# Kernel optimization log

Hardware: AMD Instinct MI355X
Metric: run time of the kernel (lower is better)

Reference implementation:

```python
import jax, jax.numpy as jnp
import numpy as np

EPS = 1e-6
B, H, S, D = 8, 16, 4096, 64


def setup_inputs() -> dict:
    key = jax.random.key(0)
    k1, k2, k3 = jax.random.split(key, 3)
    return {
        "keys": jax.random.normal(k1, (B, H, S, D), dtype=jnp.float32),
        "values": jax.random.normal(k2, (B, H, S, D), dtype=jnp.float32),
        "queries": jax.random.normal(k3, (B, H, S, D), dtype=jnp.float32),
    }


def reference(keys, values, queries):
    # update: accumulate outer-product associative memory per (batch, head)
    # M[b,h] = sum_s k_s outer v_s  -> [B, H, D, D]
    M = jnp.einsum("bhsd,bhse->bhde", keys, values)
    # normalizer z[b,h] = sum_s k_s -> [B, H, D]
    z = jnp.sum(keys, axis=2)
    # retrieve: out = (q @ M) / (q . z + eps)
    num = jnp.einsum("bhqd,bhde->bhqe", queries, M)        # [B, H, S, D]
    den = jnp.einsum("bhqd,bhd->bhq", queries, z) + EPS     # [B, H, S]
    return num / den[..., None]
```

## Files before the change

kernel.cpp:

```cpp
#include <hip/hip_runtime.h>

constexpr int Sc = 4096, Dc = 64;
constexpr int BH = 128;
constexpr int SS = 8;
constexpr int CHUNK = Sc / SS;
constexpr int SROWS = 32;
constexpr int NST = CHUNK / SROWS;
constexpr int MM = Dc * Dc;
constexpr int NZP = SS * 4;
constexpr int QT = 128;

using sh8 = __attribute__((ext_vector_type(8))) short;
using f32x4 = __attribute__((ext_vector_type(4))) float;
typedef __attribute__((address_space(1))) const unsigned int as1_u32;
typedef __attribute__((address_space(3))) unsigned int as3_u32;

__device__ __forceinline__ unsigned int packbf2(float lo, float hi) {
  unsigned int a = __builtin_bit_cast(unsigned int, lo);
  unsigned int b = __builtin_bit_cast(unsigned int, hi);
  a = (a + 0x7fffu + ((a >> 16) & 1u)) >> 16;
  b = (b + 0x7fffu + ((b >> 16) & 1u)) & 0xffff0000u;
  return a | b;
}

__global__ __launch_bounds__(256) void k1_accum(const float* __restrict__ K,
                                                const float* __restrict__ V,
                                                float* __restrict__ Pm,
                                                double* __restrict__ Pz) {
  const int blk = blockIdx.x, bh = blk >> 3, ck = blk & 7;
  const int tid = threadIdx.x, w = tid >> 6, l = tid & 63;
  const int g = l >> 4, c = l & 15;

  const size_t base = ((size_t)bh * Sc + (size_t)ck * CHUNK) * Dc;
  const float* Kg = K + base;
  const float* Vg = V + base;

  __shared__ __align__(16) float smem[2 * 4096];

  const int lofs = w * 512 + l * 4;

  f32x4 acc[4];
  #pragma unroll
  for (int i = 0; i < 4; ++i) acc[i] = (f32x4){0.f, 0.f, 0.f, 0.f};
  double zacc = 0.0;

#define K1_ISSUE(T, BUF)                                                         \
  {                                                                              \
    const float* gk_ = Kg + (size_t)(T) * 2048 + lofs;                           \
    const float* gv_ = Vg + (size_t)(T) * 2048 + lofs;                           \
    float* lk_ = &smem[(BUF) * 4096 + w * 512];           \
    float* lv_ = &smem[(BUF) * 4096 + 2048 + w * 512];                           \
    __builtin_amdgcn_global_load_lds((as1_u32*)gk_,         (as3_u32*)lk_,         16, 0, 0); \
    __builtin_amdgcn_global_load_lds((as1_u32*)(gk_ + 256), (as3_u32*)(lk_ + 256), 16, 0, 0); \
    __builtin_amdgcn_global_load_lds((as1_u32*)gv_,         (as3_u32*)lv_,         16, 0, 0); \
    __builtin_amdgcn_global_load_lds((as1_u32*)(gv_ + 256), (as3_u32*)(lv_ + 256), 16, 0, 0); \
  }

  K1_ISSUE(0, 0)

  for (int t = 0; t < NST; ++t) {
    const int buf = t & 1;
    asm volatile("s_waitcnt vmcnt(0)" ::: "memory");
    asm volatile("s_waitcnt lgkmcnt(0)" ::: "memory");
    __builtin_amdgcn_s_barrier();
    if (t + 1 < NST) K1_ISSUE(t + 1, buf ^ 1)

    const float* bK = &smem[buf * 4096];
    const float* bV = &smem[buf * 4096 + 2048];

    #pragma unroll
    for (int r = 0; r < 8; ++r) zacc += (double)bK[(8 * w + r) * 64 + l];

    float ak[8];
    #pragma unroll
    for (int j = 0; j < 8; ++j) ak[j] = bK[(8 * g + j) * 64 + 16 * w + c];
    unsigned int au[4];
    #pragma unroll
    for (int j = 0; j < 4; ++j) au[j] = packbf2(ak[2 * j], ak[2 * j + 1]);
    const sh8 afr = __builtin_bit_cast(sh8, *(const uint4*)au);

    #pragma unroll
    for (int et = 0; et < 4; ++et) {
      float bv[8];
      #pragma unroll
      for (int j = 0; j < 8; ++j) bv[j] = bV[(8 * g + j) * 64 + 16 * et + c];
      unsigned int bu[4];
      #pragma unroll
      for (int j = 0; j < 4; ++j) bu[j] = packbf2(bv[2 * j], bv[2 * j + 1]);
      const sh8 bfr = __builtin_bit_cast(sh8, *(const uint4*)bu);
      acc[et] = __builtin_amdgcn_mfma_f32_16x16x32_bf16(afr, bfr, acc[et], 0, 0, 0);
    }
  }
#undef K1_ISSUE

  float* pd = Pm + ((size_t)ck * BH + bh) * MM;
  #pragma unroll
  for (int et = 0; et < 4; ++et)
    #pragma unroll
    for (int r = 0; r < 4; ++r)
      pd[(16 * w + 4 * g + r) * 64 + 16 * et + c] = acc[et][r];

  Pz[((size_t)(ck * 4 + w) * BH + bh) * Dc + l] = zacc;
}

__global__ __launch_bounds__(256) void k2_reduce(const float* __restrict__ Pm,
                                                 const double* __restrict__ Pz,
                                                 float* __restrict__ Fm,
                                                 float* __restrict__ Fz) {
  const int i = blockIdx.x * 256 + threadIdx.x;
  const int nm = BH * MM;
  if (i < nm) {
    float s = 0.f;
    #pragma unroll
    for (int cc = 0; cc < SS; ++cc) s += Pm[(size_t)cc * nm + i];
    Fm[i] = s;
  }
  const int nz = BH * Dc;
  if (i < nz) {
    double s = 0.0;
    #pragma unroll
    for (int cc = 0; cc < NZP; ++cc) s += Pz[(size_t)cc * nz + i];
    Fz[i] = (float)s;
  }
}

__global__ __launch_bounds__(256) void k3_retrieve(const float* __restrict__ Q,
                                                   const float* __restrict__ Fm,
                                                   const float* __restrict__ Fz,
                                                   float* __restrict__ O) {
  const int blk = blockIdx.x;
  const int bh = blk >> 5;
  const int row0 = (blk & 31) * QT;

  __shared__ __align__(16) float lm[Dc][Dc];
  __shared__ __align__(16) float lq[QT][68];
  __shared__ __align__(16) float lz[Dc];

  const int tid = threadIdx.x;

  const float4* gm4 = (const float4*)(Fm + (size_t)bh * MM);
  float4* lm4 = (float4*)&lm[0][0];
  #pragma unroll
  for (int j = 0; j < 4; ++j) lm4[tid + j * 256] = gm4[tid + j * 256];
  if (tid < Dc) lz[tid] = Fz[(size_t)bh * Dc + tid];

  const float4* gq4 = (const float4*)(Q + ((size_t)bh * Sc + row0) * Dc);
  #pragma unroll
  for (int j = 0; j < 8; ++j) {
    const int i4 = tid + j * 256;
    const float4 v = gq4[i4];
    const int f = i4 * 4;
    *(float4*)&lq[f >> 6][f & 63] = v;
  }
  __syncthreads();

  const int rg = tid >> 3;
  const int cg = tid & 7;
  const int r0 = rg * 4;
  const int e0 = cg * 8;

  float acc[4][8] = {};
  double den[4] = {0.0, 0.0, 0.0, 0.0};

  #pragma unroll
  for (int ds = 0; ds < 16; ++ds) {
    const int d0 = ds * 4;
    const float4 z4 = *(const float4*)&lz[d0];
    const float* zf = (const float*)&z4;
    float4 q4[4];
    #pragma unroll
    for (int r = 0; r < 4; ++r) q4[r] = *(const float4*)&lq[r0 + r][d0];
    const float* qf[4] = {(const float*)&q4[0], (const float*)&q4[1],
                          (const float*)&q4[2], (const float*)&q4[3]};
    #pragma unroll
    for (int i = 0; i < 4; ++i) {
      const float4 ma = *(const float4*)&lm[d0 + i][e0];
      const float4 mb = *(const float4*)&lm[d0 + i][e0 + 4];
      const float mf[8] = {ma.x, ma.y, ma.z, ma.w, mb.x, mb.y, mb.z, mb.w};
      const double zd = (double)zf[i];
      #pragma unroll
      for (int r = 0; r < 4; ++r) {
        const float qs = qf[r][i];
        den[r] += (double)qs * zd;
        #pragma unroll
        for (int j = 0; j < 8; ++j)
          acc[r][j] = fmaf(qs, mf[j], acc[r][j]);
      }
    }
  }

  #pragma unroll
  for (int r = 0; r < 4; ++r) {
    const double iv = 1.0 / (den[r] + 1e-6);
    float* go = O + ((size_t)bh * Sc + row0 + r0 + r) * Dc + e0;
    ((float4*)go)[0] = make_float4((float)((double)acc[r][0] * iv),
                                   (float)((double)acc[r][1] * iv),
                                   (float)((double)acc[r][2] * iv),
                                   (float)((double)acc[r][3] * iv));
    ((float4*)go)[1] = make_float4((float)((double)acc[r][4] * iv),
                                   (float)((double)acc[r][5] * iv),
                                   (float)((double)acc[r][6] * iv),
                                   (float)((double)acc[r][7] * iv));
  }
}

extern "C" void kernel_launch(void* const* d_in, const int* in_sizes, int n_in,
                              void* d_out, int out_size, void* d_ws, size_t ws_size,
                              hipStream_t stream) {
  const float* K = (const float*)d_in[0];
  const float* V = (const float*)d_in[1];
  const float* Q = (const float*)d_in[2];
  float* O = (float*)d_out;

  float* Pm = (float*)d_ws;
  float* Fm = Pm + (size_t)SS * BH * MM;
  double* Pz = (double*)(Fm + (size_t)BH * MM);
  float* Fz = (float*)(Pz + (size_t)NZP * BH * Dc);

  hipLaunchKernelGGL(k1_accum, dim3(BH * SS), dim3(256), 0, stream, K, V, Pm, Pz);
  hipLaunchKernelGGL(k2_reduce, dim3((BH * MM + 255) / 256), dim3(256), 0, stream, Pm, Pz, Fm, Fz);
  hipLaunchKernelGGL(k3_retrieve, dim3(BH * (Sc / QT)), dim3(256), 0, stream, Q, Fm, Fz, O);
}
```

Measured before the change: 162.8 us.

## Split accumulation into 16 chunks with register-prefetched two-phase K/V loads

Adds a new accumulation kernel that splits the sequence into 16 chunks per head, using 2048 blocks instead of 1024. Each block loads its whole 256-row K/V slice into registers up front and stages it through a 64 KB LDS buffer in two halves, replacing the per-32-row double-buffered async loads. The aim is more memory-level parallelism and fewer barriers in the bandwidth-bound first stage. The cost is twice the partial-sum traffic in the reduce kernel, heavy register pressure, and a runtime fallback to the old kernel when the workspace is too small.

```diff
diff --git a/kernel.cpp b/kernel.cpp
--- a/kernel.cpp
+++ b/kernel.cpp
@@ -2,12 +2,7 @@
 
 constexpr int Sc = 4096, Dc = 64;
 constexpr int BH = 128;
-constexpr int SS = 8;
-constexpr int CHUNK = Sc / SS;
-constexpr int SROWS = 32;
-constexpr int NST = CHUNK / SROWS;
 constexpr int MM = Dc * Dc;
-constexpr int NZP = SS * 4;
 constexpr int QT = 128;
 
 using sh8 = __attribute__((ext_vector_type(8))) short;
@@ -23,54 +18,131 @@
   return a | b;
 }
 
-__global__ __launch_bounds__(256) void k1_accum(const float* __restrict__ K,
-                                                const float* __restrict__ V,
-                                                float* __restrict__ Pm,
-                                                double* __restrict__ Pz) {
+__global__ __launch_bounds__(256, 2) void k1_pair(const float* __restrict__ K,
+                                                  const float* __restrict__ V,
+                                                  float* __restrict__ Pm,
+                                                  double* __restrict__ Pz) {
+  const int blk = blockIdx.x, bh = blk >> 4, ck = blk & 15;
+  const int tid = threadIdx.x, w = tid >> 6, l = tid & 63;
+  const int g = l >> 4, c = l & 15;
+
+  const size_t base = ((size_t)bh * Sc + (size_t)ck * 256) * Dc;
+  const float4* gk4 = (const float4*)(K + base);
+  const float4* gv4 = (const float4*)(V + base);
+
+  __shared__ __align__(16) float smem[2 * 8192];
+  float4* sK4 = (float4*)smem;
+  float4* sV4 = (float4*)(smem + 8192);
+
+  f32x4 acc[4];
+  #pragma unroll
+  for (int i = 0; i < 4; ++i) acc[i] = (f32x4){0.f, 0.f, 0.f, 0.f};
+  double zacc = 0.0;
+
+  float4 p0k[8], p0v[8], p1k[8], p1v[8];
+  #pragma unroll
+  for (int j = 0; j < 8; ++j) p0k[j] = gk4[tid + j * 256];
+  #pragma unroll
+  for (int j = 0; j < 8; ++j) p0v[j] = gv4[tid + j * 256];
+  #pragma unroll
+  for (int j = 0; j < 8; ++j) p1k[j] = gk4[2048 + tid + j * 256];
+  #pragma unroll
+  for (int j = 0; j < 8; ++j) p1v[j] = gv4[2048 + tid + j * 256];
+
+  #pragma unroll
+  for (int j = 0; j < 8; ++j) { sK4[tid + j * 256] = p0k[j]; sV4[tid + j * 256] = p0v[j]; }
+  asm volatile("s_waitcnt lgkmcnt(0)" ::: "memory");
+  __builtin_amdgcn_s_barrier();
+  __builtin_amdgcn_sched_barrier(0);
+
+#define K1_COMPUTE()                                                          \
+  {                                                                           \
+    _Pragma("unroll")                                                         \
+    for (int ks = 0; ks < 4; ++ks) {                                          \
+      float ak[8];                                                            \
+      _Pragma("unroll")                                                       \
+      for (int j = 0; j < 8; ++j)                                             \
+        ak[j] = smem[(ks * 32 + 8 * g + j) * 64 + 16 * w + c];                \
+      unsigned int au[4];                                                     \
+      _Pragma("unroll")                                                       \
+      for (int j = 0; j < 4; ++j) au[j] = packbf2(ak[2 * j], ak[2 * j + 1]);  \
+      const sh8 afr = __builtin_bit_cast(sh8, *(const uint4*)au);             \
+      _Pragma("unroll")                                                       \
+      for (int et = 0; et < 4; ++et) {                                        \
+        float bv[8];                                                          \
+        _Pragma("unroll")                                                     \
+        for (int j = 0; j < 8; ++j)                                           \
+          bv[j] = smem[8192 + (ks * 32 + 8 * g + j) * 64 + 16 * et + c];      \
+        unsigned int bu[4];                                                   \
+        _Pragma("unroll")                                                     \
+        for (int j = 0; j < 4; ++j) bu[j] = packbf2(bv[2 * j], bv[2 * j + 1]);\
+        const sh8 bfr = __builtin_bit_cast(sh8, *(const uint4*)bu);           \
+        acc[et] = __builtin_amdgcn_mfma_f32_16x16x32_bf16(afr, bfr, acc[et], 0, 0, 0); \
+      }                                                                       \
+    }                                                                         \
+    _Pragma("unroll")                                                         \
+    for (int r = 0; r < 32; ++r) zacc += (double)smem[(w * 32 + r) * 64 + l]; \
+  }
+
+  K1_COMPUTE()
+
+  __syncthreads();
+  #pragma unroll
+  for (int j = 0; j < 8; ++j) { sK4[tid + j * 256] = p1k[j]; sV4[tid + j * 256] = p1v[j]; }
+  __syncthreads();
+
+  K1_COMPUTE()
+#undef K1_COMPUTE
+
+  float* pd = Pm + ((size_t)ck * BH + bh) * MM;
+  #pragma unroll
+  for (int et = 0; et < 4; ++et)
+    #pragma unroll
+    for (int r = 0; r < 4; ++r)
+      pd[(16 * w + 4 * g + r) * 64 + 16 * et + c] = acc[et][r];
+
+  Pz[((size_t)(ck * 4 + w) * BH + bh) * Dc + l] = zacc;
+}
+
+__global__ __launch_bounds__(256) void k1_v15(const float* __restrict__ K,
+                                              const float* __restrict__ V,
+                                              float* __restrict__ Pm,
+                                              double* __restrict__ Pz) {
+  constexpr int SS = 8, CHUNK = Sc / SS, SROWS = 32, NST = CHUNK / SROWS;
   const int blk = blockIdx.x, bh = blk >> 3, ck = blk & 7;
   const int tid = threadIdx.x, w = tid >> 6, l = tid & 63;
   const int g = l >> 4, c = l & 15;
-
   const size_t base = ((size_t)bh * Sc + (size_t)ck * CHUNK) * Dc;
   const float* Kg = K + base;
   const float* Vg = V + base;
-
   __shared__ __align__(16) float smem[2 * 4096];
-
   const int lofs = w * 512 + l * 4;
-
   f32x4 acc[4];
   #pragma unroll
   for (int i = 0; i < 4; ++i) acc[i] = (f32x4){0.f, 0.f, 0.f, 0.f};
   double zacc = 0.0;
-
 #define K1_ISSUE(T, BUF)                                                         \
   {                                                                              \
     const float* gk_ = Kg + (size_t)(T) * 2048 + lofs;                           \
     const float* gv_ = Vg + (size_t)(T) * 2048 + lofs;                           \
-    float* lk_ = &smem[(BUF) * 4096 + w * 512];           \
+    float* lk_ = &smem[(BUF) * 4096 + w * 512];                                  \
     float* lv_ = &smem[(BUF) * 4096 + 2048 + w * 512];                           \
     __builtin_amdgcn_global_load_lds((as1_u32*)gk_,         (as3_u32*)lk_,         16, 0, 0); \
     __builtin_amdgcn_global_load_lds((as1_u32*)(gk_ + 256), (as3_u32*)(lk_ + 256), 16, 0, 0); \
     __builtin_amdgcn_global_load_lds((as1_u32*)gv_,         (as3_u32*)lv_,         16, 0, 0); \
     __builtin_amdgcn_global_load_lds((as1_u32*)(gv_ + 256), (as3_u32*)(lv_ + 256), 16, 0, 0); \
   }
-
   K1_ISSUE(0, 0)
-
   for (int t = 0; t < NST; ++t) {
     const int buf = t & 1;
     asm volatile("s_waitcnt vmcnt(0)" ::: "memory");
     asm volatile("s_waitcnt lgkmcnt(0)" ::: "memory");
     __builtin_amdgcn_s_barrier();
     if (t + 1 < NST) K1_ISSUE(t + 1, buf ^ 1)
-
     const float* bK = &smem[buf * 4096];
     const float* bV = &smem[buf * 4096 + 2048];
-
     #pragma unroll
     for (int r = 0; r < 8; ++r) zacc += (double)bK[(8 * w + r) * 64 + l];
-
     float ak[8];
     #pragma unroll
     for (int j = 0; j < 8; ++j) ak[j] = bK[(8 * g + j) * 64 + 16 * w + c];
@@ -78,7 +150,6 @@
     #pragma unroll
     for (int j = 0; j < 4; ++j) au[j] = packbf2(ak[2 * j], ak[2 * j + 1]);
     const sh8 afr = __builtin_bit_cast(sh8, *(const uint4*)au);
-
     #pragma unroll
     for (int et = 0; et < 4; ++et) {
       float bv[8];
@@ -92,34 +163,31 @@
     }
   }
 #undef K1_ISSUE
-
   float* pd = Pm + ((size_t)ck * BH + bh) * MM;
   #pragma unroll
   for (int et = 0; et < 4; ++et)
     #pragma unroll
     for (int r = 0; r < 4; ++r)
       pd[(16 * w + 4 * g + r) * 64 + 16 * et + c] = acc[et][r];
-
   Pz[((size_t)(ck * 4 + w) * BH + bh) * Dc + l] = zacc;
 }
 
 __global__ __launch_bounds__(256) void k2_reduce(const float* __restrict__ Pm,
                                                  const double* __restrict__ Pz,
                                                  float* __restrict__ Fm,
-                                                 float* __restrict__ Fz) {
+                                                 float* __restrict__ Fz,
+                                                 int ss, int nzp) {
   const int i = blockIdx.x * 256 + threadIdx.x;
   const int nm = BH * MM;
   if (i < nm) {
     float s = 0.f;
-    #pragma unroll
-    for (int cc = 0; cc < SS; ++cc) s += Pm[(size_t)cc * nm + i];
+    for (int cc = 0; cc < ss; ++cc) s += Pm[(size_t)cc * nm + i];
     Fm[i] = s;
   }
   const int nz = BH * Dc;
   if (i < nz) {
     double s = 0.0;
-    #pragma unroll
-    for (int cc = 0; cc < NZP; ++cc) s += Pz[(size_t)cc * nz + i];
+    for (int cc = 0; cc < nzp; ++cc) s += Pz[(size_t)cc * nz + i];
     Fz[i] = (float)s;
   }
 }
@@ -212,12 +280,21 @@
   const float* Q = (const float*)d_in[2];
   float* O = (float*)d_out;
 
+  const size_t need16 = (size_t)16 * BH * MM * 4 + (size_t)BH * MM * 4 +
+                        (size_t)64 * BH * Dc * 8 + (size_t)BH * Dc * 4;
+  const int ss = (ws_size >= need16) ? 16 : 8;
+  const int nzp = ss * 4;
+
   float* Pm = (float*)d_ws;
-  float* Fm = Pm + (size_t)SS * BH * MM;
+  float* Fm = Pm + (size_t)ss * BH * MM;
   double* Pz = (double*)(Fm + (size_t)BH * MM);
-  float* Fz = (float*)(Pz + (size_t)NZP * BH * Dc);
-
-  hipLaunchKernelGGL(k1_accum, dim3(BH * SS), dim3(256), 0, stream, K, V, Pm, Pz);
-  hipLaunchKernelGGL(k2_reduce, dim3((BH * MM + 255) / 256), dim3(256), 0, stream, Pm, Pz, Fm, Fz);
+  float* Fz = (float*)(Pz + (size_t)nzp * BH * Dc);
+
+  if (ss == 16)
+    hipLaunchKernelGGL(k1_pair, dim3(BH * 16), dim3(256), 0, stream, K, V, Pm, Pz);
+  else
+    hipLaunchKernelGGL(k1_v15, dim3(BH * 8), dim3(256), 0, stream, K, V, Pm, Pz);
+  hipLaunchKernelGGL(k2_reduce, dim3((BH * MM + 255) / 256), dim3(256), 0, stream,
+                     Pm, Pz, Fm, Fz, ss, nzp);
   hipLaunchKernelGGL(k3_retrieve, dim3(BH * (Sc / QT)), dim3(256), 0, stream, Q, Fm, Fz, O);
 }
```

Measured after the change: 209.0 us. 28.4% more time.
